# Optimization experiments

Measured on AMD Instinct MI355X. Metric: run time of the kernel, lower is better.

## Reference

```python
import jax, jax.numpy as jnp
import numpy as np
import math

D_MODEL = 2048
N_HEADS = 16
D_HEAD = D_MODEL // N_HEADS
MAX_T = 2048
B, T = 2, 2048


def rotate_half(x):
    # interleaved rotate: (x0,x1,x2,x3,...) -> (-x1,x0,-x3,x2,...)
    x1 = x[..., ::2]
    x2 = x[..., 1::2]
    return jnp.stack((-x2, x1), axis=-1).reshape(x.shape)


def setup_inputs() -> dict:
    key = jax.random.key(0)
    k1, k2, k3 = jax.random.split(key, 3)
    x = jax.random.normal(k1, (B, T, D_MODEL), dtype=jnp.float32)
    # torch nn.Linear weights: [out, in]
    s = 1.0 / math.sqrt(D_MODEL)
    Wqkv = jax.random.uniform(k2, (3 * D_MODEL, D_MODEL), dtype=jnp.float32, minval=-s, maxval=s)
    WO = jax.random.uniform(k3, (D_MODEL, D_MODEL), dtype=jnp.float32, minval=-s, maxval=s)
    return {"x": x, "Wqkv": Wqkv, "WO": WO}


def reference(x, Wqkv, WO):
    Bx, Tx, _ = x.shape
    # RoPE tables (buffers)
    pos = jnp.arange(Tx, dtype=jnp.float32)
    freqs = jnp.exp(-math.log(10000.0) * jnp.arange(0, D_HEAD, 2, dtype=jnp.float32) / D_HEAD)
    angles = pos[:, None] * freqs[None, :]               # [T, d_head/2]
    sin = jnp.repeat(jnp.sin(angles), 2, axis=-1)        # [T, d_head]
    cos = jnp.repeat(jnp.cos(angles), 2, axis=-1)
    sin = sin[None, None, :, :]
    cos = cos[None, None, :, :]

    qkv = x @ Wqkv.T                                     # [B, T, 3D]
    q, k, v = jnp.split(qkv, 3, axis=-1)
    def to_heads(t):
        return t.reshape(Bx, Tx, N_HEADS, D_HEAD).transpose(0, 2, 1, 3)  # [B,H,T,d]
    q, k, v = to_heads(q), to_heads(k), to_heads(v)

    q = q * cos + rotate_half(q) * sin
    k = k * cos + rotate_half(k) * sin

    scores = jnp.einsum('bhqd,bhkd->bhqk', q, k) / math.sqrt(D_HEAD)
    mask = jnp.triu(jnp.full((Tx, Tx), -jnp.inf, dtype=scores.dtype), k=1)
    scores = scores + mask
    attn = jax.nn.softmax(scores, axis=-1)
    out = jnp.einsum('bhqk,bhkd->bhqd', attn, v)
    out = out.transpose(0, 2, 1, 3).reshape(Bx, Tx, D_MODEL)
    return out @ WO.T
```

## Files before the change

kernel.cpp:

```cpp
#include <hip/hip_runtime.h>
#include <hip/hip_bf16.h>

typedef unsigned short u16;
typedef __attribute__((ext_vector_type(8))) short bf16x8;
typedef __attribute__((ext_vector_type(4))) float f32x4;

#define B_   2
#define T_   2048
#define DM   2048
#define NH   16
#define DH   128
#define NQKV 6144

__device__ __forceinline__ u16 f2bf(float f) {
  __hip_bfloat16 h = __float2bfloat16(f);
  u16 u; __builtin_memcpy(&u, &h, 2); return u;
}
__device__ __forceinline__ float bf2f(u16 u) {
  __hip_bfloat16 h; __builtin_memcpy(&h, &u, 2); return __bfloat162float(h);
}
__device__ __forceinline__ void gl_lds16(const void* g, void* l) {
  __builtin_amdgcn_global_load_lds(
      (__attribute__((address_space(1))) unsigned int*)g,
      (__attribute__((address_space(3))) unsigned int*)l, 16, 0, 0);
}
__device__ __forceinline__ f32x4 MFMA(bf16x8 a, bf16x8 b, f32x4 c) {
  return __builtin_amdgcn_mfma_f32_16x16x32_bf16(a, b, c, 0, 0, 0);
}

__global__ __launch_bounds__(256) void cast_kernel(const float* __restrict__ in,
                                                   u16* __restrict__ out, int n4) {
  int i = blockIdx.x * 256 + threadIdx.x;
  if (i >= n4) return;
  float4 v = ((const float4*)in)[i];
  ushort4 o;
  o.x = f2bf(v.x); o.y = f2bf(v.y); o.z = f2bf(v.z); o.w = f2bf(v.w);
  ((ushort4*)out)[i] = o;
}

__global__ __launch_bounds__(256) void gemm_bt(const u16* __restrict__ A,
                                               const u16* __restrict__ Bm,
                                               void* __restrict__ Cp,
                                               int M, int N, int K, int out_f32) {
  __shared__ u16 As[128 * 64];
  __shared__ u16 Bs[128 * 64];
  const int tid  = threadIdx.x;
  const int wave = tid >> 6, lane = tid & 63;
  const int lrow = lane & 15, quad = lane >> 4;
  const long tileM = (long)blockIdx.y * 128, tileN = (long)blockIdx.x * 128;
  const int wm = (wave >> 1) * 64, wn = (wave & 1) * 64;
  const int sRowIn = lane >> 3;
  const int sChunk = (lane & 7) ^ sRowIn;
  const int sRow0  = wave * 32 + sRowIn;
  const u16* Ag = A + (tileM + sRow0) * (long)K + sChunk * 8;
  const u16* Bg = Bm + (tileN + sRow0) * (long)K + sChunk * 8;
  u16* AsW = As + wave * 2048;
  u16* BsW = Bs + wave * 2048;
  f32x4 acc[4][4] = {};
  for (int kt = 0; kt < K; kt += 64) {
#pragma unroll
    for (int i = 0; i < 4; ++i)
      gl_lds16(Ag + kt + (size_t)i * 8 * K, AsW + i * 512);
#pragma unroll
    for (int i = 0; i < 4; ++i)
      gl_lds16(Bg + kt + (size_t)i * 8 * K, BsW + i * 512);
    __syncthreads();
#pragma unroll
    for (int kb = 0; kb < 2; ++kb) {
      const int slot8 = (((kb * 4 + quad) ^ (lrow & 7)) * 8);
      bf16x8 af[4], bfr[4];
#pragma unroll
      for (int i = 0; i < 4; ++i)
        af[i]  = *(const bf16x8*)(As + (wm + i * 16 + lrow) * 64 + slot8);
#pragma unroll
      for (int i = 0; i < 4; ++i)
        bfr[i] = *(const bf16x8*)(Bs + (wn + i * 16 + lrow) * 64 + slot8);
#pragma unroll
      for (int mi = 0; mi < 4; ++mi)
#pragma unroll
        for (int ni = 0; ni < 4; ++ni)
          acc[mi][ni] = MFMA(af[mi], bfr[ni], acc[mi][ni]);
    }
    __syncthreads();
  }
  const long crow = tileM + wm + quad * 4;
  const long ccol = tileN + wn + lrow;
  if (out_f32) {
    float* C = (float*)Cp;
#pragma unroll
    for (int mi = 0; mi < 4; ++mi)
#pragma unroll
      for (int ni = 0; ni < 4; ++ni)
#pragma unroll
        for (int r = 0; r < 4; ++r)
          C[(crow + mi * 16 + r) * (long)N + (ccol + ni * 16)] = acc[mi][ni][r];
  } else {
    u16* C = (u16*)Cp;
#pragma unroll
    for (int mi = 0; mi < 4; ++mi)
#pragma unroll
      for (int ni = 0; ni < 4; ++ni)
#pragma unroll
        for (int r = 0; r < 4; ++r)
          C[(crow + mi * 16 + r) * (long)N + (ccol + ni * 16)] = f2bf(acc[mi][ni][r]);
  }
}

__global__ __launch_bounds__(256) void rope_reorder(const u16* __restrict__ qkv,
                                                    u16* __restrict__ Q,
                                                    u16* __restrict__ Kd,
                                                    u16* __restrict__ Vt) {
  const int tt = blockIdx.x;
  const int bh = blockIdx.y;
  const int b = bh >> 4, h = bh & 15;
  const int tid = threadIdx.x;
  __shared__ u16 vlds[64 * 129];
  const float qscale = 0.08838834764831845f;
#pragma unroll
  for (int it = 0; it < 16; ++it) {
    int p  = tid + it * 256;
    int tl = p >> 6;
    int i  = p & 63;
    int t  = tt * 64 + tl;
    float freq  = __expf(-9.210340371976184f * (float)i / 64.0f);
    float angle = (float)t * freq;
    float sn, cs;
    sincosf(angle, &sn, &cs);
    const u16* row = qkv + (size_t)(b * T_ + t) * NQKV;
    size_t qo = ((size_t)bh * T_ + t) * DH + 2 * i;
    float q0 = bf2f(row[h * DH + 2 * i]), q1 = bf2f(row[h * DH + 2 * i + 1]);
    Q[qo]     = f2bf((q0 * cs - q1 * sn) * qscale);
    Q[qo + 1] = f2bf((q1 * cs + q0 * sn) * qscale);
    float k0 = bf2f(row[DM + h * DH + 2 * i]), k1 = bf2f(row[DM + h * DH + 2 * i + 1]);
    Kd[qo]     = f2bf(k0 * cs - k1 * sn);
    Kd[qo + 1] = f2bf(k1 * cs + k0 * sn);
  }
#pragma unroll
  for (int it = 0; it < 32; ++it) {
    int idx = tid + it * 256;
    int tl = idx >> 7, d = idx & 127;
    vlds[tl * 129 + d] =
        qkv[(size_t)(b * T_ + tt * 64 + tl) * NQKV + 2 * DM + h * DH + d];
  }
  __syncthreads();
#pragma unroll
  for (int it = 0; it < 32; ++it) {
    int idx = tid + it * 256;
    int d = idx >> 6, tl = idx & 63;
    Vt[((size_t)bh * DH + d) * T_ + tt * 64 + tl] = vlds[tl * 129 + d];
  }
}

__global__ __launch_bounds__(256) void attn_flash(const u16* __restrict__ Q,
                                                  const u16* __restrict__ K,
                                                  const u16* __restrict__ Vt,
                                                  u16* __restrict__ AO) {
  __shared__ u16 Kl[64 * 128];
  __shared__ u16 Vl[128 * 64];
  __shared__ u16 Pl[4 * 16 * 64];
  const int pairIdx = blockIdx.x;
  const int bh = blockIdx.y;
  const int b = bh >> 4, h = bh & 15;
  const int tid = threadIdx.x;
  const int wave = tid >> 6, lane = tid & 63;
  const int lrow = lane & 15, quad = lane >> 4;
  const u16* Qb = Q + (size_t)bh * T_ * DH;
  const u16* Kb = K + (size_t)bh * T_ * DH;
  const u16* Vb = Vt + (size_t)bh * DH * T_;

  u16* KlW = Kl + wave * 2048;
  u16* VlW = Vl + wave * 2048;
  const int kRowIn = lane >> 4;
  const int vRowIn = lane >> 3;
  const int vChunk = (lane & 7) ^ vRowIn;
  u16* PlW = Pl + wave * 1024;

  for (int pass = 0; pass < 2; ++pass) {
    const int qt = pass == 0 ? (2 * gridDim.x - 1 - pairIdx) : pairIdx;
    const int qbase = qt * 64;

    bf16x8 qf[4];
    {
      const u16* qrow = Qb + (size_t)(qbase + wave * 16 + lrow) * DH + quad * 8;
#pragma unroll
      for (int kc = 0; kc < 4; ++kc) qf[kc] = *(const bf16x8*)(qrow + kc * 32);
    }
    f32x4 o[8] = {};
    float lsum[4] = {0.f, 0.f, 0.f, 0.f};

    for (int j = 0; j <= qt; ++j) {
#pragma unroll
      for (int i = 0; i < 4; ++i) {
        int krow = wave * 16 + i * 4 + kRowIn;
        int kch = (lane & 15) ^ (i * 4 + kRowIn);
        gl_lds16(Kb + (size_t)(j * 64 + krow) * DH + kch * 8, KlW + i * 512);
      }
#pragma unroll
      for (int i = 0; i < 4; ++i) {
        int vd = wave * 32 + i * 8 + vRowIn;
        gl_lds16(Vb + (size_t)vd * T_ + j * 64 + vChunk * 8, VlW + i * 512);
      }
      __syncthreads();

      f32x4 s[4] = {};
#pragma unroll
      for (int kc = 0; kc < 4; ++kc)
#pragma unroll
        for (int ns = 0; ns < 4; ++ns) {
          bf16x8 kf = *(const bf16x8*)(Kl + (ns * 16 + lrow) * 128 +
                                       (((kc * 4 + quad) ^ lrow) * 8));
          s[ns] = MFMA(qf[kc], kf, s[ns]);
        }
      if (j == qt) {
#pragma unroll
        for (int ns = 0; ns < 4; ++ns)
#pragma unroll
          for (int r = 0; r < 4; ++r)
            if (ns * 16 + lrow > wave * 16 + quad * 4 + r) s[ns][r] = -__builtin_inff();
      }
#pragma unroll
      for (int r = 0; r < 4; ++r) {
        const int prow = quad * 4 + r;
#pragma unroll
        for (int ns = 0; ns < 4; ++ns) {
          float p = __expf(s[ns][r]);
          PlW[prow * 64 + (((ns * 2 + (lrow >> 3)) ^ (prow & 7)) * 8) +
              (lrow & 7)] = f2bf(p);
          lsum[r] += p;
        }
      }

#pragma unroll
      for (int kc = 0; kc < 2; ++kc) {
        bf16x8 pf = *(const bf16x8*)(PlW + lrow * 64 +
                                     (((kc * 4 + quad) ^ (lrow & 7)) * 8));
#pragma unroll
        for (int os = 0; os < 8; ++os) {
          bf16x8 vf = *(const bf16x8*)(Vl + (os * 16 + lrow) * 64 +
                                       (((kc * 4 + quad) ^ (lrow & 7)) * 8));
          o[os] = MFMA(pf, vf, o[os]);
        }
      }
      __syncthreads();
    }
#pragma unroll
    for (int r = 0; r < 4; ++r) {
      lsum[r] += __shfl_xor(lsum[r], 1, 16);
      lsum[r] += __shfl_xor(lsum[r], 2, 16);
      lsum[r] += __shfl_xor(lsum[r], 4, 16);
      lsum[r] += __shfl_xor(lsum[r], 8, 16);
    }
#pragma unroll
    for (int r = 0; r < 4; ++r) {
      float inv = 1.0f / lsum[r];
      const size_t row = (size_t)b * T_ + qbase + wave * 16 + quad * 4 + r;
      u16* dst = AO + row * DM + h * DH;
#pragma unroll
      for (int os = 0; os < 8; ++os) dst[os * 16 + lrow] = f2bf(o[os][r] * inv);
    }
  }
}

extern "C" void kernel_launch(void* const* d_in, const int* in_sizes, int n_in,
                              void* d_out, int out_size, void* d_ws, size_t ws_size,
                              hipStream_t stream) {
  const float* x    = (const float*)d_in[0];
  const float* Wqkv = (const float*)d_in[1];
  const float* WO   = (const float*)d_in[2];
  char* ws = (char*)d_ws;
  size_t off = 0;
  u16* xb   = (u16*)(ws + off); off += (size_t)B_ * T_ * DM * 2;
  u16* wqb  = (u16*)(ws + off); off += (size_t)NQKV * DM * 2;
  u16* wob  = (u16*)(ws + off); off += (size_t)DM * DM * 2;
  u16* qkvb = (u16*)(ws + off); off += (size_t)B_ * T_ * NQKV * 2;
  u16* Qb   = (u16*)(ws + off); off += (size_t)B_ * NH * T_ * DH * 2;
  u16* Kb   = (u16*)(ws + off); off += (size_t)B_ * NH * T_ * DH * 2;
  u16* Vtb  = (u16*)(ws + off); off += (size_t)B_ * NH * T_ * DH * 2;
  u16* AO   = xb;

  cast_kernel<<<(B_ * T_ * DM / 4 + 255) / 256, 256, 0, stream>>>(x, xb, B_ * T_ * DM / 4);
  cast_kernel<<<(NQKV * DM / 4 + 255) / 256, 256, 0, stream>>>(Wqkv, wqb, NQKV * DM / 4);
  cast_kernel<<<(DM * DM / 4 + 255) / 256, 256, 0, stream>>>(WO, wob, DM * DM / 4);

  gemm_bt<<<dim3(NQKV / 128, B_ * T_ / 128), 256, 0, stream>>>(
      xb, wqb, qkvb, B_ * T_, NQKV, DM, 0);

  rope_reorder<<<dim3(T_ / 64, B_ * NH), 256, 0, stream>>>(qkvb, Qb, Kb, Vtb);

  attn_flash<<<dim3(T_ / 128, B_ * NH), 256, 0, stream>>>(Qb, Kb, Vtb, AO);

  gemm_bt<<<dim3(DM / 128, B_ * T_ / 128), 256, 0, stream>>>(
      AO, wob, d_out, B_ * T_, DM, DM, 1);
}
```

Measured before the change: 398.5 us.

## Replace QKV GEMM with 256x256-tile, 8-wave, phase-interleaved pipelined kernel

Adds a specialized QKV projection GEMM that uses 256x256 output tiles with 512 threads and double-buffered LDS. Direct global-to-LDS loads are split into quarter-stages and interleaved with four MFMA phases per K-step, with explicit barriers, vmcnt waits and setprio. The aim is to raise arithmetic intensity and hide global-load latency behind MFMA work. In exchange it uses 64KB of LDS per block, hardcodes the problem shape, and relies on fragile manual waitcnt accounting.

Measured after the change: 393.9 us. About the same (-1.2%).

```diff
diff --git a/kernel.cpp b/kernel.cpp
--- a/kernel.cpp
+++ b/kernel.cpp
@@ -36,6 +36,129 @@
   ushort4 o;
   o.x = f2bf(v.x); o.y = f2bf(v.y); o.z = f2bf(v.z); o.w = f2bf(v.w);
   ((ushort4*)out)[i] = o;
+}
+
+#define G1_M 4096
+#define G1_N 6144
+#define G1_K 2048
+
+#define MFMA_Q(AQ, M0)                                                        \
+  _Pragma("unroll") for (int e_ = 0; e_ < 2; ++e_)                            \
+  _Pragma("unroll") for (int n_ = 0; n_ < 4; ++n_)                            \
+  _Pragma("unroll") for (int kb_ = 0; kb_ < 2; ++kb_)                         \
+    acc[(M0) + e_][n_] = MFMA(AQ[e_][kb_], bfr[n_][kb_], acc[(M0) + e_][n_])
+
+#define BARRIER() asm volatile("s_barrier" ::: "memory")
+
+__global__ __launch_bounds__(512, 2) void gemm1_8ph(const u16* __restrict__ A,
+                                                    const u16* __restrict__ Bm,
+                                                    u16* __restrict__ C) {
+  __shared__ alignas(16) u16 As[2][256 * 64];
+  __shared__ alignas(16) u16 Bs[2][256 * 64];
+  const int tid = threadIdx.x;
+  const int w = tid >> 6, lane = tid & 63;
+  const int lrow = lane & 15, quad = lane >> 4;
+  const long tileM = (long)blockIdx.y * 256, tileN = (long)blockIdx.x * 256;
+  const int wm = (w >> 2) * 128, wn = (w & 3) * 64;
+
+  const int sw8 = w * 8;
+  const int srowL = lane >> 3;
+  const int schunk = ((lane & 7) ^ srowL) * 8;
+  const u16* Ag0 = A + (tileM + sw8 + srowL) * (long)G1_K + schunk;
+  const u16* Bg0 = Bm + (tileN + sw8 + srowL) * (long)G1_K + schunk;
+
+  auto stgA = [&](int tt, int h) {
+    const int b = tt & 1;
+    gl_lds16(Ag0 + (size_t)(h * 128) * G1_K + tt * 64,
+             &As[b][(h * 128 + sw8) * 64]);
+    gl_lds16(Ag0 + (size_t)(h * 128 + 64) * G1_K + tt * 64,
+             &As[b][(h * 128 + 64 + sw8) * 64]);
+  };
+  auto stgB = [&](int tt, int h) {
+    const int b = tt & 1;
+    gl_lds16(Bg0 + (size_t)(h * 128) * G1_K + tt * 64,
+             &Bs[b][(h * 128 + sw8) * 64]);
+    gl_lds16(Bg0 + (size_t)(h * 128 + 64) * G1_K + tt * 64,
+             &Bs[b][(h * 128 + 64 + sw8) * 64]);
+  };
+
+  const int aBase = (wm + lrow) * 64;
+  const int bBase = (wn + lrow) * 64;
+  const int slot[2] = { (quad ^ (lrow & 7)) * 8, ((4 + quad) ^ (lrow & 7)) * 8 };
+
+  f32x4 acc[8][4] = {};
+
+  stgA(0, 0); stgA(0, 1); stgB(0, 0); stgB(0, 1);
+  stgB(1, 0); stgB(1, 1); stgA(1, 0);
+  asm volatile("s_waitcnt vmcnt(6)" ::: "memory");
+  BARRIER();
+
+#pragma unroll 1
+  for (int t = 0; t < 32; ++t) {
+    const u16* AsC = As[t & 1];
+    const u16* BsC = Bs[t & 1];
+    bf16x8 a01[2][2], a23[2][2], a45[2][2], a67[2][2], bfr[4][2];
+#pragma unroll
+    for (int e = 0; e < 2; ++e)
+#pragma unroll
+      for (int kb = 0; kb < 2; ++kb)
+        a01[e][kb] = *(const bf16x8*)(AsC + aBase + e * 1024 + slot[kb]);
+#pragma unroll
+    for (int ni = 0; ni < 4; ++ni)
+#pragma unroll
+      for (int kb = 0; kb < 2; ++kb)
+        bfr[ni][kb] = *(const bf16x8*)(BsC + bBase + ni * 1024 + slot[kb]);
+#pragma unroll
+    for (int e = 0; e < 2; ++e)
+#pragma unroll
+      for (int kb = 0; kb < 2; ++kb)
+        a23[e][kb] = *(const bf16x8*)(AsC + aBase + (2 + e) * 1024 + slot[kb]);
+    if (t + 1 < 32) stgA(t + 1, 1);
+    BARRIER();
+    __builtin_amdgcn_s_setprio(1);
+    MFMA_Q(a01, 0);
+    __builtin_amdgcn_s_setprio(0);
+    BARRIER();
+#pragma unroll
+    for (int e = 0; e < 2; ++e)
+#pragma unroll
+      for (int kb = 0; kb < 2; ++kb) {
+        a45[e][kb] = *(const bf16x8*)(AsC + aBase + (4 + e) * 1024 + slot[kb]);
+        a67[e][kb] = *(const bf16x8*)(AsC + aBase + (6 + e) * 1024 + slot[kb]);
+      }
+    if (t + 2 < 32) stgB(t + 2, 0);
+    BARRIER();
+    __builtin_amdgcn_s_setprio(1);
+    MFMA_Q(a23, 2);
+    __builtin_amdgcn_s_setprio(0);
+    asm volatile("s_waitcnt lgkmcnt(0)" ::: "memory");
+    BARRIER();
+    if (t + 2 < 32) stgB(t + 2, 1);
+    BARRIER();
+    __builtin_amdgcn_s_setprio(1);
+    MFMA_Q(a45, 4);
+    __builtin_amdgcn_s_setprio(0);
+    BARRIER();
+    if (t + 2 < 32) stgA(t + 2, 0);
+    if (t < 30) { asm volatile("s_waitcnt vmcnt(6)" ::: "memory"); }
+    else if (t == 30) { asm volatile("s_waitcnt vmcnt(0)" ::: "memory"); }
+    BARRIER();
+    __builtin_amdgcn_s_setprio(1);
+    MFMA_Q(a67, 6);
+    __builtin_amdgcn_s_setprio(0);
+    BARRIER();
+  }
+
+  const long crow = tileM + wm + quad * 4;
+  const long ccol = tileN + wn + lrow;
+#pragma unroll
+  for (int mi = 0; mi < 8; ++mi)
+#pragma unroll
+    for (int ni = 0; ni < 4; ++ni)
+#pragma unroll
+      for (int r = 0; r < 4; ++r)
+        C[(crow + mi * 16 + r) * (long)G1_N + (ccol + ni * 16)] =
+            f2bf(acc[mi][ni][r]);
 }
 
 __global__ __launch_bounds__(256) void gemm_bt(const u16* __restrict__ A,
@@ -282,8 +405,7 @@
   cast_kernel<<<(NQKV * DM / 4 + 255) / 256, 256, 0, stream>>>(Wqkv, wqb, NQKV * DM / 4);
   cast_kernel<<<(DM * DM / 4 + 255) / 256, 256, 0, stream>>>(WO, wob, DM * DM / 4);
 
-  gemm_bt<<<dim3(NQKV / 128, B_ * T_ / 128), 256, 0, stream>>>(
-      xb, wqb, qkvb, B_ * T_, NQKV, DM, 0);
+  gemm1_8ph<<<dim3(G1_N / 256, G1_M / 256), 512, 0, stream>>>(xb, wqb, qkvb);
 
   rope_reorder<<<dim3(T_ / 64, B_ * NH), 256, 0, stream>>>(qkvb, Qb, Kb, Vtb);
 
```
